# Optimization experiments

Hardware: AMD Instinct MI355X
Metric: run time of the kernel (lower is better)

## Reference

```python
import jax, jax.numpy as jnp
import numpy as np
from jax import lax

NUM_CHANNELS = 3
NUM_HEADS = 8
PATCH = 16  # projection_dim = 3 * 16 * 16 = 768
EPS = 1e-5


def setup_inputs() -> dict:
    key = jax.random.key(0)
    ks = jax.random.split(key, 16)
    B, N, D, Hdim = 4, 1024, 768, 3072
    H = NUM_HEADS

    def init(k, shape, fan_in):
        bound = 1.0 / np.sqrt(fan_in)
        return jax.random.uniform(k, shape, jnp.float32, -bound, bound)

    return {
        "x": jax.random.normal(ks[0], (B, N, D), jnp.float32),
        # 3x3 conv QKV projections over per-patch [3,16,16] images (no bias, qkv_bias=False)
        "qconv_w": init(ks[1], (NUM_CHANNELS, NUM_CHANNELS, 3, 3), NUM_CHANNELS * 9),
        "kconv_w": init(ks[2], (NUM_CHANNELS, NUM_CHANNELS, 3, 3), NUM_CHANNELS * 9),
        "vconv_w": init(ks[3], (NUM_CHANNELS, NUM_CHANNELS, 3, 3), NUM_CHANNELS * 9),
        # 1x1 conv mixing heads of the attention map + BatchNorm2d(heads)
        "reatten_w": init(ks[4], (H, H), H),
        "reatten_b": init(ks[5], (H,), H),
        "bn_g": jnp.ones((H,), jnp.float32),
        "bn_b": jnp.zeros((H,), jnp.float32),
        # output projection (Linear dim->dim)
        "proj_w": init(ks[6], (D, D), D),
        "proj_b": init(ks[7], (D,), D),
        # LayerNorm over (num_patches, projection_dim) jointly
        "ln_g": jnp.ones((N, D), jnp.float32),
        "ln_b": jnp.zeros((N, D), jnp.float32),
        # FeedForward
        "ff_w1": init(ks[8], (Hdim, D), D),
        "ff_b1": init(ks[9], (Hdim,), D),
        "ff_w2": init(ks[10], (D, Hdim), Hdim),
        "ff_b2": init(ks[11], (D,), Hdim),
    }


def _conv3x3(x, w):
    # x: [BN, C, p, p], w: [C, C, 3, 3], stride 1, SAME padding
    return lax.conv_general_dilated(x, w, (1, 1), "SAME",
                                    dimension_numbers=("NCHW", "OIHW", "NCHW"))


def _layernorm_2d(x, g, b):
    # LayerNorm over last two axes (N, D) jointly, biased variance, eps=1e-5
    mu = jnp.mean(x, axis=(-2, -1), keepdims=True)
    var = jnp.mean(jnp.square(x - mu), axis=(-2, -1), keepdims=True)
    return (x - mu) * lax.rsqrt(var + EPS) * g + b


def _encoder_fwd(x, qconv_w, kconv_w, vconv_w, reatten_w, reatten_b,
                 bn_g, bn_b, proj_w, proj_b, ln_g, ln_b,
                 ff_w1, ff_b1, ff_w2, ff_b2):
    B, N, D = x.shape
    H = NUM_HEADS
    hd = D // H
    scale = hd ** -0.5

    # --- ReAttention ---
    xi = x.reshape(B * N, NUM_CHANNELS, PATCH, PATCH)

    def qkv(w):
        y = _conv3x3(xi, w).reshape(B, N, H, hd)
        return y.transpose(0, 2, 1, 3)  # [B, H, N, hd]

    q, k, v = qkv(qconv_w), qkv(kconv_w), qkv(vconv_w)

    attn = jax.nn.softmax(jnp.einsum("bhnd,bhmd->bhnm", q, k) * scale, axis=-1)

    # learned cross-head 1x1 conv + BatchNorm2d (training-mode batch stats)
    attn = jnp.einsum("gh,bhnm->bgnm", reatten_w, attn) + reatten_b[None, :, None, None]
    mu = jnp.mean(attn, axis=(0, 2, 3), keepdims=True)
    var = jnp.mean(jnp.square(attn - mu), axis=(0, 2, 3), keepdims=True)
    attn = (attn - mu) * lax.rsqrt(var + EPS)
    attn = attn * bn_g[None, :, None, None] + bn_b[None, :, None, None]

    out = jnp.einsum("bhnm,bhmd->bhnd", attn, v)
    out = out.transpose(0, 2, 1, 3).reshape(B, N, D)
    out = out @ proj_w.T + proj_b

    # --- residual + LN ---
    x1 = _layernorm_2d(x + out, ln_g, ln_b)

    # --- FeedForward (exact GELU) + residual + LN ---
    h = jax.nn.gelu(x1 @ ff_w1.T + ff_b1, approximate=False)
    ff = h @ ff_w2.T + ff_b2
    return _layernorm_2d(x1 + ff, ln_g, ln_b)


def reference(x, qconv_w, kconv_w, vconv_w, reatten_w, reatten_b,
              bn_g, bn_b, proj_w, proj_b, ln_g, ln_b,
              ff_w1, ff_b1, ff_w2, ff_b2):
    return _encoder_fwd(x, qconv_w, kconv_w, vconv_w, reatten_w, reatten_b,
                        bn_g, bn_b, proj_w, proj_b, ln_g, ln_b,
                        ff_w1, ff_b1, ff_w2, ff_b2)
```

## Files before the change

kernel.cpp:

```cpp
#include <hip/hip_runtime.h>
#include <math.h>


typedef unsigned short u16;
typedef unsigned int u32;
typedef __bf16 bf16x8 __attribute__((ext_vector_type(8)));
typedef float f32x4 __attribute__((ext_vector_type(4)));

#define EPSV 1e-5f
#define SL2E 0.14724444620253177f
#define EXPC -11.541560327111707f

__device__ __forceinline__ u16 f2bf(float f) {
  union { float f; u32 u; } v; v.f = f;
  u32 u = v.u + 0x7fffu + ((v.u >> 16) & 1u);
  return (u16)(u >> 16);
}
__device__ __forceinline__ float bf2f(u16 h) {
  union { u32 u; float f; } v; v.u = ((u32)h) << 16; return v.f;
}
__device__ __forceinline__ f32x4 mfma16(bf16x8 a, bf16x8 b, f32x4 c) {
  return __builtin_amdgcn_mfma_f32_16x16x32_bf16(a, b, c, 0, 0, 0);
}
__device__ __forceinline__ void gload16(const void* gp, void* lp) {
  __builtin_amdgcn_global_load_lds(
      (const __attribute__((address_space(1))) u32*)gp,
      (__attribute__((address_space(3))) u32*)lp, 16, 0, 0);
}

struct KS { int off[3]; int hl[3]; };
__device__ __forceinline__ KS ks_init(int t) {
  KS ks;
  int lane = t & 63;
  int lh = lane >> 4, l15 = lane & 15;
  #pragma unroll
  for (int j = 0; j < 3; ++j) {
    int G = j * 512 + t;
    int hl = (G >= 768) ? 1 : 0;
    int C = (G - hl * 768) >> 6;
    int chunk = C / 6, r = C - 6 * chunk;
    int kk = r >> 1, c1 = r & 1;
    int m = chunk * 32 + ((l15 >> 2) << 3) + (c1 << 2) + (l15 & 3);
    ks.off[j] = m * 96 + kk * 32 + lh * 8;
    ks.hl[j] = hl;
  }
  return ks;
}
__device__ __forceinline__ void ks_stage(const u16* __restrict__ khi,
    const u16* __restrict__ klo, size_t rowel, const KS& ks, u16* Kb, int t) {
  int w = t >> 6;
  #pragma unroll
  for (int j = 0; j < 3; ++j) {
    const u16* src = (ks.hl[j] ? klo : khi) + rowel + ks.off[j];
    gload16(src, Kb + (size_t)(j * 512 + w * 64) * 8);
  }
}

__device__ __forceinline__ void qload(const u16* __restrict__ qhi,
    const u16* __restrict__ qlo, size_t qoff, bf16x8* qh, bf16x8* ql) {
  #pragma unroll
  for (int kk = 0; kk < 3; ++kk) {
    qh[kk] = *(const bf16x8*)(qhi + qoff + kk * 32);
    ql[kk] = *(const bf16x8*)(qlo + qoff + kk * 32);
  }
}

__device__ __forceinline__ void score18(const u16* Kb, int mh, int lane,
    const bf16x8* qh, const bf16x8* ql, f32x4& C0, f32x4& C1) {
  C0 = (f32x4){0.f, 0.f, 0.f, 0.f};
  C1 = (f32x4){0.f, 0.f, 0.f, 0.f};
  #pragma unroll
  for (int kk = 0; kk < 3; ++kk) {
    const u16* base = Kb + (mh * 6 + kk * 2) * 512 + lane * 8;
    bf16x8 kh0 = *(const bf16x8*)(base);
    bf16x8 kh1 = *(const bf16x8*)(base + 512);
    bf16x8 kl0 = *(const bf16x8*)(base + 6144);
    bf16x8 kl1 = *(const bf16x8*)(base + 6656);
    C0 = mfma16(kh0, qh[kk], C0);
    C0 = mfma16(kl0, qh[kk], C0);
    C0 = mfma16(kh0, ql[kk], C0);
    C1 = mfma16(kh1, qh[kk], C1);
    C1 = mfma16(kl1, qh[kk], C1);
    C1 = mfma16(kh1, ql[kk], C1);
  }
}

__global__ __launch_bounds__(256) void k_f2b(const float* __restrict__ s,
                                             u16* __restrict__ d, int n) {
  int i = blockIdx.x * 256 + threadIdx.x;
  int stride = gridDim.x * 256;
  for (; i < n; i += stride) d[i] = f2bf(s[i]);
}

__global__ __launch_bounds__(256) void k_conv(const float* __restrict__ x,
    const float* __restrict__ wq, const float* __restrict__ wk, const float* __restrict__ wv,
    u16* __restrict__ qhi, u16* __restrict__ qlo,
    u16* __restrict__ khi, u16* __restrict__ klo,
    float* __restrict__ vb)
{
  __shared__ float patch[768], swq[81], swk[81], swv[81];
  int bid = blockIdx.x;
  int b = bid >> 10, n = bid & 1023;
  int t = threadIdx.x;
  const float* xr = x + (size_t)bid * 768;
  patch[t] = xr[t]; patch[t + 256] = xr[t + 256]; patch[t + 512] = xr[t + 512];
  if (t < 81) { swq[t] = wq[t]; swk[t] = wk[t]; swv[t] = wv[t]; }
  __syncthreads();
  #pragma unroll
  for (int r = 0; r < 3; ++r) {
    int f = t + 256 * r;
    int o = f >> 8, rem = f & 255, pp = rem >> 4, qq = rem & 15;
    float aq = 0.f, ak = 0.f, av = 0.f;
    #pragma unroll
    for (int i = 0; i < 3; ++i)
      #pragma unroll
      for (int dp = 0; dp < 3; ++dp) {
        int ip = pp + dp - 1;
        if (ip < 0 || ip > 15) continue;
        #pragma unroll
        for (int dq = 0; dq < 3; ++dq) {
          int iq = qq + dq - 1;
          if (iq < 0 || iq > 15) continue;
          float pv = patch[i * 256 + ip * 16 + iq];
          int wi = ((o * 3 + i) * 3 + dp) * 3 + dq;
          aq += swq[wi] * pv; ak += swk[wi] * pv; av += swv[wi] * pv;
        }
      }
    int h = f / 96, d = f - h * 96;
    size_t oi = ((size_t)(b * 8 + h) * 1024 + n) * 96 + d;
    float aqs = aq * SL2E;
    u16 qh_ = f2bf(aqs); qhi[oi] = qh_; qlo[oi] = f2bf(aqs - bf2f(qh_));
    u16 kh_ = f2bf(ak);  khi[oi] = kh_; klo[oi] = f2bf(ak - bf2f(kh_));
    vb[oi] = av;
  }
}

__global__ __launch_bounds__(256) void k_vtr(const float* __restrict__ vb,
                                             u16* __restrict__ vtr)
{
  __shared__ u16 lds[12288];
  int bid = blockIdx.x;
  int bh = bid >> 3, n0 = (bid & 7) * 128;
  int t = threadIdx.x;
  int n = t >> 1, dh = (t & 1) * 48;
  const float* src = vb + ((size_t)bh * 1024 + n0 + n) * 96 + dh;
  #pragma unroll
  for (int j4 = 0; j4 < 12; ++j4) {
    float4 v = *(const float4*)(src + j4 * 4);
    int d = dh + j4 * 4;
    lds[(d + 0) * 128 + n] = f2bf(v.x);
    lds[(d + 1) * 128 + n] = f2bf(v.y);
    lds[(d + 2) * 128 + n] = f2bf(v.z);
    lds[(d + 3) * 128 + n] = f2bf(v.w);
  }
  __syncthreads();
  #pragma unroll
  for (int j = 0; j < 48; ++j) {
    int flat = t + 256 * j;
    int d = flat >> 7, n2 = flat & 127;
    vtr[((size_t)bh * 96 + d) * 1024 + n0 + n2] = lds[flat];
  }
}

__global__ __launch_bounds__(512, 2) void k_score(
    const u16* __restrict__ qhi, const u16* __restrict__ qlo,
    const u16* __restrict__ khi, const u16* __restrict__ klo,
    float* __restrict__ zp, u16* __restrict__ pt)
{
  __shared__ u16 Kst[2][12288];
  int p = blockIdx.x;
  int s = p >> 3;
  int c = (p & 7) * 4 + (s >> 4);
  int ng = s & 15;
  int b = c >> 3, mg = c & 7;
  int t = threadIdx.x, lane = t & 63, w = t >> 6;
  int l15 = lane & 15, lhi = lane >> 4;
  int nsub = w >> 1, mh = w & 1;
  int n0 = ng * 64 + nsub * 16;
  int nt = ng * 4 + nsub;
  int m0base = mg * 128;
  KS ks = ks_init(t);
  bf16x8 qh[3], ql[3], qh2[3], ql2[3];
  size_t bh0 = (size_t)(b * 8) * 1024;
  ks_stage(khi, klo, (bh0 + m0base) * 96, ks, Kst[0], t);
  qload(qhi, qlo, (bh0 + n0 + l15) * 96 + lhi * 8, qh, ql);
  __syncthreads();
  #pragma unroll 1
  for (int h = 0; h < 8; ++h) {
    float z = 0.f;
    #pragma unroll
    for (int mt = 0; mt < 2; ++mt) {
      int u = h * 2 + mt;
      if (u < 15) {
        int un = u + 1, hn = un >> 1, mtn = un & 1;
        size_t bhn = (size_t)(b * 8 + hn) * 1024;
        ks_stage(khi, klo, (bhn + m0base + mtn * 64) * 96, ks, Kst[(u + 1) & 1], t);
        if (mtn == 0)
          qload(qhi, qlo, (bhn + n0 + l15) * 96 + lhi * 8, qh2, ql2);
      }
      f32x4 C0, C1;
      score18(Kst[u & 1], mh, lane, qh, ql, C0, C1);
      union { u16 us[8]; uint4 q4; } pk;
      #pragma unroll
      for (int r = 0; r < 4; ++r) {
        float e0 = exp2f(C0[r] + EXPC);
        float e1 = exp2f(C1[r] + EXPC);
        z += e0 + e1;
        pk.us[r]     = f2bf(e0);
        pk.us[4 + r] = f2bf(e1);
      }
      int mc = mg * 4 + mt * 2 + mh;
      *(uint4*)&pt[((((size_t)(b * 8 + h) * 32 + mc) * 64 + nt) * 64 + lane) * 8] = pk.q4;
      if (u < 15 && mt == 1) {
        #pragma unroll
        for (int kk = 0; kk < 3; ++kk) { qh[kk] = qh2[kk]; ql[kk] = ql2[kk]; }
      }
      __syncthreads();
    }
    z += __shfl_xor(z, 16);
    z += __shfl_xor(z, 32);
    if (lane < 16)
      zp[((size_t)((b * 8 + h) * 16 + mg * 2 + mh)) * 1024 + n0 + lane] = z;
  }
}

__global__ __launch_bounds__(256) void k_zmerge(const float* __restrict__ zp,
                                                float* __restrict__ invZ)
{
  int idx = blockIdx.x * 256 + threadIdx.x;
  int bh = idx >> 10, n = idx & 1023;
  float z = 0.f;
  #pragma unroll
  for (int s = 0; s < 16; ++s) z += zp[((size_t)(bh * 16 + s)) * 1024 + n];
  invZ[idx] = 1.f / z;
}

__global__ __launch_bounds__(512, 2) void k_mixpv(
    const u16* __restrict__ pt, const u16* __restrict__ vtr,
    const float* __restrict__ invZ, const float* __restrict__ rw,
    float* __restrict__ U, float* __restrict__ pstat)
{
  __shared__ u16 Pst[2][8192];
  int p = blockIdx.x;
  int xcd = p & 7;
  int b = xcd >> 1, nt = (xcd & 1) * 32 + (p >> 3);
  int t = threadIdx.x, lane = t & 63, w = t >> 6;
  int l15 = lane & 15, lhi = lane >> 4;

  float wg[8]; float wsum = 0.f;
  #pragma unroll
  for (int h = 0; h < 8; ++h) { wg[h] = rw[w * 8 + h]; wsum += wg[h]; }
  float cg = -wsum * (1.f / 1024.f);
  float wz[8];
  #pragma unroll
  for (int h = 0; h < 8; ++h)
    wz[h] = wg[h] * invZ[(b * 8 + h) * 1024 + nt * 16 + l15];

  f32x4 acc[6];
  #pragma unroll
  for (int ds = 0; ds < 6; ++ds) acc[ds] = (f32x4){0.f, 0.f, 0.f, 0.f};
  float sc = 0.f, scc = 0.f;
  size_t vbase = (size_t)(b * 8 + w) * 96;
  size_t pbase = ((size_t)(b * 8 + w) * 32) * 4096 + (size_t)nt * 64;

  gload16(pt + (pbase + lane) * 8, &Pst[0][(size_t)t * 8]);
  __syncthreads();
  #pragma unroll 1
  for (int mc = 0; mc < 32; ++mc) {
    if (mc < 31)
      gload16(pt + (pbase + (size_t)(mc + 1) * 4096 + lane) * 8,
              &Pst[(mc + 1) & 1][(size_t)t * 8]);
    int mof = mc * 32 + lhi * 8;
    bf16x8 vf[6];
    #pragma unroll
    for (int ds = 0; ds < 6; ++ds)
      vf[ds] = *(const bf16x8*)(vtr + (vbase + ds * 16 + l15) * 1024 + mof);
    float cm8[8];
    #pragma unroll
    for (int j = 0; j < 8; ++j) cm8[j] = cg;
    const u16* Pb = &Pst[mc & 1][0];
    #pragma unroll
    for (int h = 0; h < 8; ++h) {
      union { u32 ud[4]; bf16x8 bv; } pf;
      pf.bv = *(const bf16x8*)&Pb[(h * 64 + lane) * 8];
      float wzh = wz[h];
      #pragma unroll
      for (int k2 = 0; k2 < 4; ++k2) {
        union { u32 u; float f; } lo, hi;
        lo.u = pf.ud[k2] << 16;
        hi.u = pf.ud[k2] & 0xffff0000u;
        cm8[2 * k2]     += wzh * lo.f;
        cm8[2 * k2 + 1] += wzh * hi.f;
      }
    }
    union { u16 us[8]; bf16x8 bv; } pk2;
    #pragma unroll
    for (int j = 0; j < 8; ++j) {
      sc += cm8[j]; scc += cm8[j] * cm8[j];
      pk2.us[j] = f2bf(cm8[j]);
    }
    #pragma unroll
    for (int ds = 0; ds < 6; ++ds)
      acc[ds] = mfma16(pk2.bv, vf[ds], acc[ds]);
    __syncthreads();
  }

  #pragma unroll
  for (int off = 32; off > 0; off >>= 1) {
    sc += __shfl_down(sc, off); scc += __shfl_down(scc, off);
  }
  if (lane == 0) { pstat[p * 16 + w] = sc; pstat[p * 16 + 8 + w] = scc; }

  #pragma unroll
  for (int ds = 0; ds < 6; ++ds)
    #pragma unroll
    for (int r = 0; r < 4; ++r) {
      int n = nt * 16 + lhi * 4 + r;
      U[((size_t)(b * 1024 + n)) * 768 + w * 96 + ds * 16 + l15] = acc[ds][r];
    }
}

__global__ __launch_bounds__(384) void k_vcs(const float* __restrict__ vb,
                                             float* __restrict__ vcs)
{
  __shared__ float part[4][96];
  int bh = blockIdx.x, t = threadIdx.x;
  int c = t % 96, g4 = t / 96;
  float a = 0.f;
  const float* vp = vb + (size_t)bh * 98304 + (size_t)g4 * 24576 + c;
  for (int m = 0; m < 256; ++m) a += vp[m * 96];
  part[g4][c] = a;
  __syncthreads();
  if (t < 96) vcs[bh * 96 + t] = part[0][t] + part[1][t] + part[2][t] + part[3][t];
}

__global__ __launch_bounds__(256) void k_statred(const float* __restrict__ pstat,
                                                 float* __restrict__ stats)
{
  __shared__ float part[16][17];
  int t = threadIdx.x;
  int j = t >> 4, s = t & 15;
  float a = 0.f;
  #pragma unroll
  for (int k2 = 0; k2 < 16; ++k2)
    a += pstat[(size_t)(s + 16 * k2) * 16 + j];
  part[j][s] = a;
  __syncthreads();
  if (t < 16) {
    float v = 0.f;
    #pragma unroll
    for (int s2 = 0; s2 < 16; ++s2) v += part[t][s2];
    stats[t] = v;
  }
}

__global__ __launch_bounds__(256) void k_bnfin(const float* __restrict__ U,
    const float* __restrict__ vcs, const float* __restrict__ stats,
    const float* __restrict__ bng, const float* __restrict__ bnb,
    u16* __restrict__ ubb)
{
  size_t idx = (size_t)blockIdx.x * 256 + threadIdx.x;
  int col = (int)(idx % 768); int i = (int)(idx / 768); int b = i >> 10;
  int g = col / 96, d = col - g * 96;
  const float cnt = 4194304.f;
  float mc = stats[g] / cnt;
  float var = stats[8 + g] / cnt - mc * mc;
  float sg = bng[g] * rsqrtf(var + EPSV);
  float tg = bnb[g] - sg * mc;
  ubb[idx] = f2bf(sg * U[idx] + tg * vcs[(b * 8 + g) * 96 + d]);
}

template<int GELU_, int RES_, int STATS_, int BF16OUT>
__global__ __launch_bounds__(256) void k_gemm(
    const u16* __restrict__ A, const u16* __restrict__ W,
    const float* __restrict__ bias, const float* __restrict__ res,
    float* __restrict__ out, u16* __restrict__ outb,
    int K, int Nc, float* __restrict__ stats)
{
  __shared__ u16 As[8192], Bs[8192];
  __shared__ float red[8];
  int t = threadIdx.x, lane = t & 63, wv = t >> 6;
  int l15 = lane & 15, lhi = lane >> 4;
  int i0 = blockIdx.y * 128, j0 = blockIdx.x * 128;
  int wr = wv >> 1, wc = wv & 1;
  f32x4 acc[4][4];
  #pragma unroll
  for (int mi = 0; mi < 4; ++mi)
    #pragma unroll
    for (int ni = 0; ni < 4; ++ni) acc[mi][ni] = (f32x4){0.f, 0.f, 0.f, 0.f};
  int rA = lane >> 3;
  int colel = 8 * ((lane & 7) ^ rA);
  for (int k0 = 0; k0 < K; k0 += 64) {
    if (k0) __syncthreads();
    #pragma unroll
    for (int i = 0; i < 4; ++i) {
      int cA = wv * 4 + i;
      int r = cA * 8 + rA;
      gload16(A + (size_t)(i0 + r) * K + k0 + colel, &As[cA * 512]);
      gload16(W + (size_t)(j0 + r) * K + k0 + colel, &Bs[cA * 512]);
    }
    __syncthreads();
    #pragma unroll
    for (int ks = 0; ks < 2; ++ks) {
      bf16x8 af[4], bf[4];
      #pragma unroll
      for (int mi = 0; mi < 4; ++mi) {
        int r2 = wr * 64 + mi * 16 + l15;
        af[mi] = *(const bf16x8*)&As[r2 * 64 + ((ks * 32 + lhi * 8) ^ (8 * (r2 & 7)))];
      }
      #pragma unroll
      for (int ni = 0; ni < 4; ++ni) {
        int r3 = wc * 64 + ni * 16 + l15;
        bf[ni] = *(const bf16x8*)&Bs[r3 * 64 + ((ks * 32 + lhi * 8) ^ (8 * (r3 & 7)))];
      }
      #pragma unroll
      for (int mi = 0; mi < 4; ++mi)
        #pragma unroll
        for (int ni = 0; ni < 4; ++ni)
          acc[mi][ni] = mfma16(af[mi], bf[ni], acc[mi][ni]);
    }
  }
  float ls = 0.f, lss = 0.f;
  #pragma unroll
  for (int mi = 0; mi < 4; ++mi) {
    #pragma unroll
    for (int ni = 0; ni < 4; ++ni) {
      int col = j0 + wc * 64 + ni * 16 + l15;
      float bv = bias[col];
      #pragma unroll
      for (int r = 0; r < 4; ++r) {
        int row = i0 + wr * 64 + mi * 16 + lhi * 4 + r;
        float val = acc[mi][ni][r] + bv;
        if (RES_) val += res[(size_t)row * Nc + col];
        if (GELU_) val = 0.5f * val * (1.f + erff(val * 0.70710678118654752f));
        if (BF16OUT) outb[(size_t)row * Nc + col] = f2bf(val);
        else out[(size_t)row * Nc + col] = val;
        if (STATS_) { ls += val; lss += val * val; }
      }
    }
  }
  if (STATS_) {
    #pragma unroll
    for (int off = 32; off > 0; off >>= 1) {
      ls += __shfl_down(ls, off); lss += __shfl_down(lss, off);
    }
    if (lane == 0) { red[wv * 2] = ls; red[wv * 2 + 1] = lss; }
    __syncthreads();
    if (t == 0) {
      int b = i0 >> 10;
      atomicAdd(&stats[b * 2],     red[0] + red[2] + red[4] + red[6]);
      atomicAdd(&stats[b * 2 + 1], red[1] + red[3] + red[5] + red[7]);
    }
  }
}

template<int BF16OUT>
__global__ __launch_bounds__(256) void k_ln(const float* __restrict__ y,
    const float* __restrict__ stats, const float* __restrict__ g,
    const float* __restrict__ bta, float* __restrict__ outp, u16* __restrict__ outb)
{
  size_t idx = (size_t)blockIdx.x * 256 + threadIdx.x;
  int i = (int)(idx / 768), col = (int)(idx % 768);
  int b = i >> 10, n = i & 1023;
  const float cnt = 786432.f;
  float mu = stats[b * 2] / cnt;
  float var = stats[b * 2 + 1] / cnt - mu * mu;
  float r = rsqrtf(var + EPSV);
  size_t gi = (size_t)n * 768 + col;
  float v = (y[idx] - mu) * r * g[gi] + bta[gi];
  outp[idx] = v;
  if (BF16OUT) outb[idx] = f2bf(v);
}

extern "C" void kernel_launch(void* const* d_in, const int* in_sizes, int n_in,
                              void* d_out, int out_size, void* d_ws, size_t ws_size,
                              hipStream_t stream)
{
  const float* x   = (const float*)d_in[0];
  const float* qw  = (const float*)d_in[1];
  const float* kw  = (const float*)d_in[2];
  const float* vw  = (const float*)d_in[3];
  const float* rw  = (const float*)d_in[4];
  const float* bng = (const float*)d_in[6];
  const float* bnb = (const float*)d_in[7];
  const float* pw  = (const float*)d_in[8];
  const float* pb  = (const float*)d_in[9];
  const float* lng = (const float*)d_in[10];
  const float* lnb = (const float*)d_in[11];
  const float* fw1 = (const float*)d_in[12];
  const float* fb1 = (const float*)d_in[13];
  const float* fw2 = (const float*)d_in[14];
  const float* fb2 = (const float*)d_in[15];
  float* out = (float*)d_out;

  u16* pt   = (u16*)d_ws;
  float* vb = (float*)pt;
  u16* hb   = pt;
  float* y2 = (float*)pt + 12582912;
  float* fsm = (float*)(pt + 33554432);
  float* stats = fsm;
  float* pstat = fsm + 64;
  float* vcs   = fsm + 4160;
  float* zp    = fsm + 7232;
  float* invZ  = fsm + 531520;
  u16* qhi  = (u16*)(fsm + 564288);
  u16* qlo  = qhi + 3145728;
  u16* khi  = qlo + 3145728;
  u16* klo  = khi + 3145728;
  u16* vtrb = klo + 3145728;
  u16* pwb  = vtrb + 3145728;
  u16* fw1b = pwb + 589824;
  u16* fw2b = fw1b + 2359296;
  float* U0 = (float*)qhi;
  float* x1 = (float*)khi;
  float* y1 = U0;
  u16* ubb  = vtrb;
  u16* x1b  = vtrb;

  hipMemsetAsync(stats, 0, 64 * sizeof(float), stream);
  k_f2b<<<1024, 256, 0, stream>>>(pw, pwb, 589824);
  k_f2b<<<2048, 256, 0, stream>>>(fw1, fw1b, 2359296);
  k_f2b<<<2048, 256, 0, stream>>>(fw2, fw2b, 2359296);

  k_conv<<<4096, 256, 0, stream>>>(x, qw, kw, vw, qhi, qlo, khi, klo, vb);
  k_vtr<<<256, 256, 0, stream>>>(vb, vtrb);
  k_vcs<<<32, 384, 0, stream>>>(vb, vcs);
  k_score<<<512, 512, 0, stream>>>(qhi, qlo, khi, klo, zp, pt);
  k_zmerge<<<128, 256, 0, stream>>>(zp, invZ);
  k_mixpv<<<256, 512, 0, stream>>>(pt, vtrb, invZ, rw, U0, pstat);
  k_statred<<<1, 256, 0, stream>>>(pstat, stats);
  k_bnfin<<<12288, 256, 0, stream>>>(U0, vcs, stats, bng, bnb, ubb);

  k_gemm<0,1,1,0><<<dim3(6, 32), 256, 0, stream>>>(ubb, pwb, pb, x, y1, nullptr, 768, 768, stats + 16);
  k_ln<1><<<12288, 256, 0, stream>>>(y1, stats + 16, lng, lnb, x1, x1b);
  k_gemm<1,0,0,1><<<dim3(24, 32), 256, 0, stream>>>(x1b, fw1b, fb1, nullptr, nullptr, hb, 768, 3072, nullptr);
  k_gemm<0,1,1,0><<<dim3(6, 32), 256, 0, stream>>>(hb, fw2b, fb2, x1, y2, nullptr, 3072, 768, stats + 24);
  k_ln<0><<<12288, 256, 0, stream>>>(y2, stats + 24, lng, lnb, out, nullptr);
}
```

Before: 299.5 us.

## Split mixpv key dimension across two blocks and drop LDS staging

The mix-PV kernel now splits the 1024-key reduction into two halves handled by separate blocks, doubling the grid to 512 blocks. Each half writes a partial U buffer, and the BN finalize kernel sums the two partials. The LDS double-buffer and per-iteration __syncthreads are replaced by direct per-thread global vector loads of P, with unroll 2 to overlap loads. The aim is more parallelism and less sync overhead, at the cost of an extra full-size fp32 partial write and read, and of reusing the khi buffer as U1.

```diff
diff --git a/kernel.cpp b/kernel.cpp
--- a/kernel.cpp
+++ b/kernel.cpp
@@ -238,12 +238,13 @@
 __global__ __launch_bounds__(512, 2) void k_mixpv(
     const u16* __restrict__ pt, const u16* __restrict__ vtr,
     const float* __restrict__ invZ, const float* __restrict__ rw,
-    float* __restrict__ U, float* __restrict__ pstat)
-{
-  __shared__ u16 Pst[2][8192];
+    float* __restrict__ U0, float* __restrict__ U1,
+    float* __restrict__ pstat)
+{
   int p = blockIdx.x;
   int xcd = p & 7;
-  int b = xcd >> 1, nt = (xcd & 1) * 32 + (p >> 3);
+  int b = xcd >> 1, mhf = xcd & 1;
+  int nt = p >> 3;
   int t = threadIdx.x, lane = t & 63, w = t >> 6;
   int l15 = lane & 15, lhi = lane >> 4;
 
@@ -261,15 +262,14 @@
   for (int ds = 0; ds < 6; ++ds) acc[ds] = (f32x4){0.f, 0.f, 0.f, 0.f};
   float sc = 0.f, scc = 0.f;
   size_t vbase = (size_t)(b * 8 + w) * 96;
-  size_t pbase = ((size_t)(b * 8 + w) * 32) * 4096 + (size_t)nt * 64;
-
-  gload16(pt + (pbase + lane) * 8, &Pst[0][(size_t)t * 8]);
-  __syncthreads();
-  #pragma unroll 1
-  for (int mc = 0; mc < 32; ++mc) {
-    if (mc < 31)
-      gload16(pt + (pbase + (size_t)(mc + 1) * 4096 + lane) * 8,
-              &Pst[(mc + 1) & 1][(size_t)t * 8]);
+  size_t phb = ((size_t)(b * 8) * 32) * 4096 + (size_t)nt * 64 + lane;
+
+  #pragma unroll 2
+  for (int mc = mhf * 16; mc < mhf * 16 + 16; ++mc) {
+    bf16x8 pf[8];
+    #pragma unroll
+    for (int h = 0; h < 8; ++h)
+      pf[h] = *(const bf16x8*)(pt + (phb + (size_t)h * 131072 + (size_t)mc * 4096) * 8);
     int mof = mc * 32 + lhi * 8;
     bf16x8 vf[6];
     #pragma unroll
@@ -278,17 +278,16 @@
     float cm8[8];
     #pragma unroll
     for (int j = 0; j < 8; ++j) cm8[j] = cg;
-    const u16* Pb = &Pst[mc & 1][0];
     #pragma unroll
     for (int h = 0; h < 8; ++h) {
-      union { u32 ud[4]; bf16x8 bv; } pf;
-      pf.bv = *(const bf16x8*)&Pb[(h * 64 + lane) * 8];
+      union { u32 ud[4]; bf16x8 bv; } pu;
+      pu.bv = pf[h];
       float wzh = wz[h];
       #pragma unroll
       for (int k2 = 0; k2 < 4; ++k2) {
         union { u32 u; float f; } lo, hi;
-        lo.u = pf.ud[k2] << 16;
-        hi.u = pf.ud[k2] & 0xffff0000u;
+        lo.u = pu.ud[k2] << 16;
+        hi.u = pu.ud[k2] & 0xffff0000u;
         cm8[2 * k2]     += wzh * lo.f;
         cm8[2 * k2 + 1] += wzh * hi.f;
       }
@@ -302,7 +301,6 @@
     #pragma unroll
     for (int ds = 0; ds < 6; ++ds)
       acc[ds] = mfma16(pk2.bv, vf[ds], acc[ds]);
-    __syncthreads();
   }
 
   #pragma unroll
@@ -311,12 +309,13 @@
   }
   if (lane == 0) { pstat[p * 16 + w] = sc; pstat[p * 16 + 8 + w] = scc; }
 
+  float* Uq = mhf ? U1 : U0;
   #pragma unroll
   for (int ds = 0; ds < 6; ++ds)
     #pragma unroll
     for (int r = 0; r < 4; ++r) {
       int n = nt * 16 + lhi * 4 + r;
-      U[((size_t)(b * 1024 + n)) * 768 + w * 96 + ds * 16 + l15] = acc[ds][r];
+      Uq[((size_t)(b * 1024 + n)) * 768 + w * 96 + ds * 16 + l15] = acc[ds][r];
     }
 }
 
@@ -342,7 +341,7 @@
   int j = t >> 4, s = t & 15;
   float a = 0.f;
   #pragma unroll
-  for (int k2 = 0; k2 < 16; ++k2)
+  for (int k2 = 0; k2 < 32; ++k2)
     a += pstat[(size_t)(s + 16 * k2) * 16 + j];
   part[j][s] = a;
   __syncthreads();
@@ -354,10 +353,10 @@
   }
 }
 
-__global__ __launch_bounds__(256) void k_bnfin(const float* __restrict__ U,
-    const float* __restrict__ vcs, const float* __restrict__ stats,
-    const float* __restrict__ bng, const float* __restrict__ bnb,
-    u16* __restrict__ ubb)
+__global__ __launch_bounds__(256) void k_bnfin(const float* __restrict__ U0,
+    const float* __restrict__ U1, const float* __restrict__ vcs,
+    const float* __restrict__ stats, const float* __restrict__ bng,
+    const float* __restrict__ bnb, u16* __restrict__ ubb)
 {
   size_t idx = (size_t)blockIdx.x * 256 + threadIdx.x;
   int col = (int)(idx % 768); int i = (int)(idx / 768); int b = i >> 10;
@@ -367,7 +366,7 @@
   float var = stats[8 + g] / cnt - mc * mc;
   float sg = bng[g] * rsqrtf(var + EPSV);
   float tg = bnb[g] - sg * mc;
-  ubb[idx] = f2bf(sg * U[idx] + tg * vcs[(b * 8 + g) * 96 + d]);
+  ubb[idx] = f2bf(sg * (U0[idx] + U1[idx]) + tg * vcs[(b * 8 + g) * 96 + d]);
 }
 
 template<int GELU_, int RES_, int STATS_, int BF16OUT>
@@ -500,10 +499,10 @@
   float* fsm = (float*)(pt + 33554432);
   float* stats = fsm;
   float* pstat = fsm + 64;
-  float* vcs   = fsm + 4160;
-  float* zp    = fsm + 7232;
-  float* invZ  = fsm + 531520;
-  u16* qhi  = (u16*)(fsm + 564288);
+  float* vcs   = fsm + 8256;
+  float* zp    = fsm + 11328;
+  float* invZ  = fsm + 535616;
+  u16* qhi  = (u16*)(fsm + 568384);
   u16* qlo  = qhi + 3145728;
   u16* khi  = qlo + 3145728;
   u16* klo  = khi + 3145728;
@@ -512,6 +511,7 @@
   u16* fw1b = pwb + 589824;
   u16* fw2b = fw1b + 2359296;
   float* U0 = (float*)qhi;
+  float* U1 = (float*)khi;
   float* x1 = (float*)khi;
   float* y1 = U0;
   u16* ubb  = vtrb;
@@ -527,9 +527,9 @@
   k_vcs<<<32, 384, 0, stream>>>(vb, vcs);
   k_score<<<512, 512, 0, stream>>>(qhi, qlo, khi, klo, zp, pt);
   k_zmerge<<<128, 256, 0, stream>>>(zp, invZ);
-  k_mixpv<<<256, 512, 0, stream>>>(pt, vtrb, invZ, rw, U0, pstat);
+  k_mixpv<<<512, 512, 0, stream>>>(pt, vtrb, invZ, rw, U0, U1, pstat);
   k_statred<<<1, 256, 0, stream>>>(pstat, stats);
-  k_bnfin<<<12288, 256, 0, stream>>>(U0, vcs, stats, bng, bnb, ubb);
+  k_bnfin<<<12288, 256, 0, stream>>>(U0, U1, vcs, stats, bng, bnb, ubb);
 
   k_gemm<0,1,1,0><<<dim3(6, 32), 256, 0, stream>>>(ubb, pwb, pb, x, y1, nullptr, 768, 768, stats + 16);
   k_ln<1><<<12288, 256, 0, stream>>>(y1, stats + 16, lng, lnb, x1, x1b);
```

Measured after the change: 302.5 us. About the same (+1.0%).

## Split fused head-mix/PV kernel into separate in-place mix and PV kernels

Applied to the files above, without the earlier changes.

Replaces the fused k_mixpv kernel (256 blocks of 512 threads, each wave mixing all 8 heads through LDS double-buffering before an MFMA against V) with two kernels. k_mix applies the cross-head 1x1 mix in place on the bf16 probability buffer across 2048 blocks and writes per-block BN partial stats. k_pv then runs a plain P·V MFMA per (batch, head-group, row tile). The aim is more parallelism and occupancy, at the cost of one extra full read and write of the 64MB P buffer, an extra launch, and a larger stats reduction.

```diff
diff --git a/kernel.cpp b/kernel.cpp
--- a/kernel.cpp
+++ b/kernel.cpp
@@ -235,88 +235,121 @@
   invZ[idx] = 1.f / z;
 }
 
-__global__ __launch_bounds__(512, 2) void k_mixpv(
+__global__ __launch_bounds__(256, 4) void k_mix(
+    u16* __restrict__ pt, const float* __restrict__ invZ,
+    const float* __restrict__ rw, float* __restrict__ pstat)
+{
+  __shared__ float red[4][16];
+  int t = threadIdx.x;
+  int gid = blockIdx.x * 256 + t;
+  int lane = gid & 63;
+  int nt = (gid >> 6) & 63;
+  int mc = (gid >> 12) & 31;
+  int b  = gid >> 17;
+  int n = nt * 16 + (lane & 15);
+  float iz[8];
+  #pragma unroll
+  for (int h = 0; h < 8; ++h) iz[h] = invZ[(b * 8 + h) * 1024 + n];
+  float out[8][8];
+  #pragma unroll
+  for (int g = 0; g < 8; ++g) {
+    float wsum = 0.f;
+    #pragma unroll
+    for (int h = 0; h < 8; ++h) wsum += rw[g * 8 + h];
+    float cg = -wsum * (1.f / 1024.f);
+    #pragma unroll
+    for (int e = 0; e < 8; ++e) out[g][e] = cg;
+  }
+  size_t base = ((((size_t)(b * 8) * 32 + mc) * 64 + nt) * 64 + lane) * 8;
+  #pragma unroll
+  for (int h = 0; h < 8; ++h) {
+    union { u32 ud[4]; uint4 q; } gr;
+    gr.q = *(const uint4*)(pt + base + (size_t)h * 1048576);
+    float q[8];
+    #pragma unroll
+    for (int k2 = 0; k2 < 4; ++k2) {
+      union { u32 u; float f; } lo, hi;
+      lo.u = gr.ud[k2] << 16;
+      hi.u = gr.ud[k2] & 0xffff0000u;
+      q[2 * k2]     = lo.f * iz[h];
+      q[2 * k2 + 1] = hi.f * iz[h];
+    }
+    #pragma unroll
+    for (int g = 0; g < 8; ++g) {
+      float wgh = rw[g * 8 + h];
+      #pragma unroll
+      for (int e = 0; e < 8; ++e) out[g][e] += wgh * q[e];
+    }
+  }
+  float sc[8], scc[8];
+  #pragma unroll
+  for (int g = 0; g < 8; ++g) {
+    float s = 0.f, ss = 0.f;
+    union { u16 us[8]; uint4 q; } pk;
+    #pragma unroll
+    for (int e = 0; e < 8; ++e) {
+      float v = out[g][e];
+      s += v; ss += v * v;
+      pk.us[e] = f2bf(v);
+    }
+    sc[g] = s; scc[g] = ss;
+    *(uint4*)(pt + base + (size_t)g * 1048576) = pk.q;
+  }
+  int wv = t >> 6, lane2 = t & 63;
+  #pragma unroll
+  for (int off = 32; off > 0; off >>= 1)
+    #pragma unroll
+    for (int g = 0; g < 8; ++g) {
+      sc[g] += __shfl_down(sc[g], off);
+      scc[g] += __shfl_down(scc[g], off);
+    }
+  if (lane2 == 0) {
+    #pragma unroll
+    for (int g = 0; g < 8; ++g) {
+      red[wv][g] = sc[g];
+      red[wv][8 + g] = scc[g];
+    }
+  }
+  __syncthreads();
+  if (t < 16)
+    pstat[(size_t)blockIdx.x * 16 + t] =
+        red[0][t] + red[1][t] + red[2][t] + red[3][t];
+}
+
+__global__ __launch_bounds__(256, 4) void k_pv(
     const u16* __restrict__ pt, const u16* __restrict__ vtr,
-    const float* __restrict__ invZ, const float* __restrict__ rw,
-    float* __restrict__ U, float* __restrict__ pstat)
-{
-  __shared__ u16 Pst[2][8192];
+    float* __restrict__ U)
+{
   int p = blockIdx.x;
-  int xcd = p & 7;
-  int b = xcd >> 1, nt = (xcd & 1) * 32 + (p >> 3);
   int t = threadIdx.x, lane = t & 63, w = t >> 6;
   int l15 = lane & 15, lhi = lane >> 4;
-
-  float wg[8]; float wsum = 0.f;
-  #pragma unroll
-  for (int h = 0; h < 8; ++h) { wg[h] = rw[w * 8 + h]; wsum += wg[h]; }
-  float cg = -wsum * (1.f / 1024.f);
-  float wz[8];
-  #pragma unroll
-  for (int h = 0; h < 8; ++h)
-    wz[h] = wg[h] * invZ[(b * 8 + h) * 1024 + nt * 16 + l15];
-
+  int xcd = p & 7;
+  int i = p >> 3;
+  int pair = xcd * 4 + (i >> 4);
+  int ntq = i & 15;
+  int b = pair >> 3, g = pair & 7;
+  int nt = ntq * 4 + w;
   f32x4 acc[6];
   #pragma unroll
   for (int ds = 0; ds < 6; ++ds) acc[ds] = (f32x4){0.f, 0.f, 0.f, 0.f};
-  float sc = 0.f, scc = 0.f;
-  size_t vbase = (size_t)(b * 8 + w) * 96;
-  size_t pbase = ((size_t)(b * 8 + w) * 32) * 4096 + (size_t)nt * 64;
-
-  gload16(pt + (pbase + lane) * 8, &Pst[0][(size_t)t * 8]);
-  __syncthreads();
-  #pragma unroll 1
+  size_t pbase = ((((size_t)(b * 8 + g) * 32) * 64 + nt) * 64 + lane);
+  size_t vbase = (size_t)(b * 8 + g) * 96;
+  #pragma unroll 2
   for (int mc = 0; mc < 32; ++mc) {
-    if (mc < 31)
-      gload16(pt + (pbase + (size_t)(mc + 1) * 4096 + lane) * 8,
-              &Pst[(mc + 1) & 1][(size_t)t * 8]);
+    bf16x8 pf = *(const bf16x8*)(pt + (pbase + (size_t)mc * 4096) * 8);
     int mof = mc * 32 + lhi * 8;
-    bf16x8 vf[6];
-    #pragma unroll
-    for (int ds = 0; ds < 6; ++ds)
-      vf[ds] = *(const bf16x8*)(vtr + (vbase + ds * 16 + l15) * 1024 + mof);
-    float cm8[8];
-    #pragma unroll
-    for (int j = 0; j < 8; ++j) cm8[j] = cg;
-    const u16* Pb = &Pst[mc & 1][0];
-    #pragma unroll
-    for (int h = 0; h < 8; ++h) {
-      union { u32 ud[4]; bf16x8 bv; } pf;
-      pf.bv = *(const bf16x8*)&Pb[(h * 64 + lane) * 8];
-      float wzh = wz[h];
-      #pragma unroll
-      for (int k2 = 0; k2 < 4; ++k2) {
-        union { u32 u; float f; } lo, hi;
-        lo.u = pf.ud[k2] << 16;
-        hi.u = pf.ud[k2] & 0xffff0000u;
-        cm8[2 * k2]     += wzh * lo.f;
-        cm8[2 * k2 + 1] += wzh * hi.f;
-      }
-    }
-    union { u16 us[8]; bf16x8 bv; } pk2;
-    #pragma unroll
-    for (int j = 0; j < 8; ++j) {
-      sc += cm8[j]; scc += cm8[j] * cm8[j];
-      pk2.us[j] = f2bf(cm8[j]);
-    }
-    #pragma unroll
-    for (int ds = 0; ds < 6; ++ds)
-      acc[ds] = mfma16(pk2.bv, vf[ds], acc[ds]);
-    __syncthreads();
-  }
-
-  #pragma unroll
-  for (int off = 32; off > 0; off >>= 1) {
-    sc += __shfl_down(sc, off); scc += __shfl_down(scc, off);
-  }
-  if (lane == 0) { pstat[p * 16 + w] = sc; pstat[p * 16 + 8 + w] = scc; }
-
+    #pragma unroll
+    for (int ds = 0; ds < 6; ++ds) {
+      bf16x8 vf = *(const bf16x8*)(vtr + (vbase + ds * 16 + l15) * 1024 + mof);
+      acc[ds] = mfma16(pf, vf, acc[ds]);
+    }
+  }
   #pragma unroll
   for (int ds = 0; ds < 6; ++ds)
     #pragma unroll
     for (int r = 0; r < 4; ++r) {
       int n = nt * 16 + lhi * 4 + r;
-      U[((size_t)(b * 1024 + n)) * 768 + w * 96 + ds * 16 + l15] = acc[ds][r];
+      U[((size_t)(b * 1024 + n)) * 768 + g * 96 + ds * 16 + l15] = acc[ds][r];
     }
 }
 
@@ -341,8 +374,7 @@
   int t = threadIdx.x;
   int j = t >> 4, s = t & 15;
   float a = 0.f;
-  #pragma unroll
-  for (int k2 = 0; k2 < 16; ++k2)
+  for (int k2 = 0; k2 < 128; ++k2)
     a += pstat[(size_t)(s + 16 * k2) * 16 + j];
   part[j][s] = a;
   __syncthreads();
@@ -500,10 +532,10 @@
   float* fsm = (float*)(pt + 33554432);
   float* stats = fsm;
   float* pstat = fsm + 64;
-  float* vcs   = fsm + 4160;
-  float* zp    = fsm + 7232;
-  float* invZ  = fsm + 531520;
-  u16* qhi  = (u16*)(fsm + 564288);
+  float* vcs   = fsm + 32832;
+  float* zp    = fsm + 35904;
+  float* invZ  = fsm + 560192;
+  u16* qhi  = (u16*)(fsm + 592960);
   u16* qlo  = qhi + 3145728;
   u16* khi  = qlo + 3145728;
   u16* klo  = khi + 3145728;
@@ -527,7 +559,8 @@
   k_vcs<<<32, 384, 0, stream>>>(vb, vcs);
   k_score<<<512, 512, 0, stream>>>(qhi, qlo, khi, klo, zp, pt);
   k_zmerge<<<128, 256, 0, stream>>>(zp, invZ);
-  k_mixpv<<<256, 512, 0, stream>>>(pt, vtrb, invZ, rw, U0, pstat);
+  k_mix<<<2048, 256, 0, stream>>>(pt, invZ, rw, pstat);
+  k_pv<<<512, 256, 0, stream>>>(pt, vtrb, U0);
   k_statred<<<1, 256, 0, stream>>>(pstat, stats);
   k_bnfin<<<12288, 256, 0, stream>>>(U0, vcs, stats, bng, bnb, ubb);
 
```

New measurement: 367.4 us. +22.7%, slower.

## Split-K the second feed-forward GEMM into three partials with a fused reduce kernel

Applied to the files above, without the earlier changes.

Replaces the single FF2 GEMM, which launched only 192 blocks, with a three-way split-K GEMM writing fp32 partials, followed by a kernel that sums the partials, adds bias and residual, and accumulates the LayerNorm statistics. This raises block count to better fill the GPU's compute units. The trade-off is extra global memory traffic for the partial buffers plus one more kernel launch.

```diff
diff --git a/kernel.cpp b/kernel.cpp
--- a/kernel.cpp
+++ b/kernel.cpp
@@ -454,6 +454,99 @@
   }
 }
 
+__global__ __launch_bounds__(256) void k_gemm_part(
+    const u16* __restrict__ A, const u16* __restrict__ W,
+    float* __restrict__ P, int K, int KSfull, int Nc)
+{
+  __shared__ u16 As[8192], Bs[8192];
+  int t = threadIdx.x, lane = t & 63, wv = t >> 6;
+  int l15 = lane & 15, lhi = lane >> 4;
+  int i0 = blockIdx.y * 128, j0 = blockIdx.x * 128;
+  int kz = blockIdx.z;
+  int kbase = kz * K;
+  float* out = P + (size_t)kz * 4096 * Nc;
+  int wr = wv >> 1, wc = wv & 1;
+  f32x4 acc[4][4];
+  #pragma unroll
+  for (int mi = 0; mi < 4; ++mi)
+    #pragma unroll
+    for (int ni = 0; ni < 4; ++ni) acc[mi][ni] = (f32x4){0.f, 0.f, 0.f, 0.f};
+  int rA = lane >> 3;
+  int colel = 8 * ((lane & 7) ^ rA);
+  for (int k0 = 0; k0 < K; k0 += 64) {
+    if (k0) __syncthreads();
+    #pragma unroll
+    for (int i = 0; i < 4; ++i) {
+      int cA = wv * 4 + i;
+      int r = cA * 8 + rA;
+      gload16(A + (size_t)(i0 + r) * KSfull + kbase + k0 + colel, &As[cA * 512]);
+      gload16(W + (size_t)(j0 + r) * KSfull + kbase + k0 + colel, &Bs[cA * 512]);
+    }
+    __syncthreads();
+    #pragma unroll
+    for (int ks = 0; ks < 2; ++ks) {
+      bf16x8 af[4], bf[4];
+      #pragma unroll
+      for (int mi = 0; mi < 4; ++mi) {
+        int r2 = wr * 64 + mi * 16 + l15;
+        af[mi] = *(const bf16x8*)&As[r2 * 64 + ((ks * 32 + lhi * 8) ^ (8 * (r2 & 7)))];
+      }
+      #pragma unroll
+      for (int ni = 0; ni < 4; ++ni) {
+        int r3 = wc * 64 + ni * 16 + l15;
+        bf[ni] = *(const bf16x8*)&Bs[r3 * 64 + ((ks * 32 + lhi * 8) ^ (8 * (r3 & 7)))];
+      }
+      #pragma unroll
+      for (int mi = 0; mi < 4; ++mi)
+        #pragma unroll
+        for (int ni = 0; ni < 4; ++ni)
+          acc[mi][ni] = mfma16(af[mi], bf[ni], acc[mi][ni]);
+    }
+  }
+  #pragma unroll
+  for (int mi = 0; mi < 4; ++mi)
+    #pragma unroll
+    for (int ni = 0; ni < 4; ++ni) {
+      int col = j0 + wc * 64 + ni * 16 + l15;
+      #pragma unroll
+      for (int r = 0; r < 4; ++r) {
+        int row = i0 + wr * 64 + mi * 16 + lhi * 4 + r;
+        out[(size_t)row * Nc + col] = acc[mi][ni][r];
+      }
+    }
+}
+
+__global__ __launch_bounds__(256) void k_fin2(const float* __restrict__ P,
+    const float* __restrict__ bias, const float* __restrict__ res,
+    float* __restrict__ y, float* __restrict__ stats)
+{
+  __shared__ float red[8];
+  size_t base = (size_t)blockIdx.x * 3072;
+  int b = (int)(base / 786432);
+  int t = threadIdx.x;
+  float ls = 0.f, lss = 0.f;
+  #pragma unroll
+  for (int j = 0; j < 12; ++j) {
+    size_t idx = base + t + j * 256;
+    int col = (int)(idx % 768);
+    float v = (P[idx] + P[idx + 3145728]) + (P[idx + 6291456] + bias[col]) +
+              res[idx];
+    y[idx] = v;
+    ls += v; lss += v * v;
+  }
+  int lane = t & 63, wv = t >> 6;
+  #pragma unroll
+  for (int off = 32; off > 0; off >>= 1) {
+    ls += __shfl_down(ls, off); lss += __shfl_down(lss, off);
+  }
+  if (lane == 0) { red[wv * 2] = ls; red[wv * 2 + 1] = lss; }
+  __syncthreads();
+  if (t == 0) {
+    atomicAdd(&stats[b * 2],     red[0] + red[2] + red[4] + red[6]);
+    atomicAdd(&stats[b * 2 + 1], red[1] + red[3] + red[5] + red[7]);
+  }
+}
+
 template<int BF16OUT>
 __global__ __launch_bounds__(256) void k_ln(const float* __restrict__ y,
     const float* __restrict__ stats, const float* __restrict__ g,
@@ -496,7 +589,7 @@
   u16* pt   = (u16*)d_ws;
   float* vb = (float*)pt;
   u16* hb   = pt;
-  float* y2 = (float*)pt + 12582912;
+  float* pfin = (float*)(pt + 12582912);
   float* fsm = (float*)(pt + 33554432);
   float* stats = fsm;
   float* pstat = fsm + 64;
@@ -514,6 +607,7 @@
   float* U0 = (float*)qhi;
   float* x1 = (float*)khi;
   float* y1 = U0;
+  float* y2 = U0;
   u16* ubb  = vtrb;
   u16* x1b  = vtrb;
 
@@ -534,6 +628,7 @@
   k_gemm<0,1,1,0><<<dim3(6, 32), 256, 0, stream>>>(ubb, pwb, pb, x, y1, nullptr, 768, 768, stats + 16);
   k_ln<1><<<12288, 256, 0, stream>>>(y1, stats + 16, lng, lnb, x1, x1b);
   k_gemm<1,0,0,1><<<dim3(24, 32), 256, 0, stream>>>(x1b, fw1b, fb1, nullptr, nullptr, hb, 768, 3072, nullptr);
-  k_gemm<0,1,1,0><<<dim3(6, 32), 256, 0, stream>>>(hb, fw2b, fb2, x1, y2, nullptr, 3072, 768, stats + 24);
+  k_gemm_part<<<dim3(6, 32, 3), 256, 0, stream>>>(hb, fw2b, pfin, 1024, 3072, 768);
+  k_fin2<<<1024, 256, 0, stream>>>(pfin, fb2, x1, y2, stats + 24);
   k_ln<0><<<12288, 256, 0, stream>>>(y2, stats + 24, lng, lnb, out, nullptr);
 }
```

New measurement: 306.7 us. 1.02x slower.
